# Performance work log

Hardware: AMD Instinct MI355X
Metric: run time of the kernel (lower is better)

## Reference

```python
import jax, jax.numpy as jnp
import numpy as np

TEMPERATURE = 0.1
EPS = 1e-12  # matches F.normalize eps clamp


def setup_inputs() -> dict:
    key = jax.random.key(0)
    k1, k2 = jax.random.split(key)
    B, D = 4096, 1024
    z1 = jax.random.normal(k1, (B, D), dtype=jnp.float32)
    z2 = jax.random.normal(k2, (B, D), dtype=jnp.float32)
    return {"z1": z1, "z2": z2}


def reference(z1, z2):
    B = z1.shape[0]
    # L2-normalize rows (F.normalize dim=1, eps clamp)
    n1 = z1 / jnp.maximum(jnp.linalg.norm(z1, axis=1, keepdims=True), EPS)
    n2 = z2 / jnp.maximum(jnp.linalg.norm(z2, axis=1, keepdims=True), EPS)
    reps = jnp.concatenate([n1, n2], axis=0)  # [2B, D]
    # Rows are unit-norm, so cosine similarity == dot product -> one GEMM
    sim = (reps @ reps.T) / TEMPERATURE  # [2B, 2B]
    # positives: diag offsets +B and -B
    pos = jnp.concatenate([jnp.diagonal(sim, B), jnp.diagonal(sim, -B)])  # [2B]
    # logits row i = [pos_i, sim[i, j != i]]. logsumexp over that set =
    # logaddexp(pos_i, logsumexp over the row with the main diagonal removed).
    eye = jnp.eye(2 * B, dtype=bool)
    masked = jnp.where(eye, -jnp.inf, sim)
    lse_neg = jax.scipy.special.logsumexp(masked, axis=1)  # [2B]
    lse = jnp.logaddexp(pos, lse_neg)
    # CrossEntropyLoss with labels==0 -> mean(lse - logit_0) = mean(lse - pos)
    return jnp.mean(lse - pos)
```

## Files before the change

kernel.cpp:

```cpp
#include <hip/hip_runtime.h>

#define D_DIM 1024
#define B_HALF 4096
#define NROWS 8192
#define INV_T8 (10.0f / 256.0f)
#define NKT64 16
#define NBIG 512
#define NBLK 576

typedef float floatx4 __attribute__((ext_vector_type(4)));

#define MFMA8 __builtin_amdgcn_mfma_f32_16x16x32_fp8_fp8
#define AS1 const __attribute__((address_space(1))) unsigned int*
#define AS3 __attribute__((address_space(3))) unsigned int*

__global__ __launch_bounds__(256) void normalize_kernel(
    const float* __restrict__ z1, const float* __restrict__ z2,
    unsigned char* __restrict__ R8, float* __restrict__ S)
{
    const int tid = threadIdx.x;
    const int lane = tid & 63;
    const int row = blockIdx.x * 4 + (tid >> 6);
    const float* src = (row < B_HALF) ? (z1 + (size_t)row * D_DIM)
                                      : (z2 + (size_t)(row - B_HALF) * D_DIM);
    const float4* s4 = (const float4*)src;
    float4 v0 = s4[lane], v1 = s4[64 + lane], v2 = s4[128 + lane], v3 = s4[192 + lane];
    if (lane == 0) S[row] = 0.0f;
    float ss = v0.x*v0.x + v0.y*v0.y + v0.z*v0.z + v0.w*v0.w
             + v1.x*v1.x + v1.y*v1.y + v1.z*v1.z + v1.w*v1.w
             + v2.x*v2.x + v2.y*v2.y + v2.z*v2.z + v2.w*v2.w
             + v3.x*v3.x + v3.y*v3.y + v3.z*v3.z + v3.w*v3.w;
    ss += __shfl_xor(ss, 1);
    ss += __shfl_xor(ss, 2);
    ss += __shfl_xor(ss, 4);
    ss += __shfl_xor(ss, 8);
    ss += __shfl_xor(ss, 16);
    ss += __shfl_xor(ss, 32);
    float scale = 16.0f / fmaxf(sqrtf(ss), 1e-12f);
    int* dst = (int*)(R8 + (size_t)row * D_DIM);
    float4 vv[4] = {v0, v1, v2, v3};
    #pragma unroll
    for (int i = 0; i < 4; ++i) {
        int w = __builtin_amdgcn_cvt_pk_fp8_f32(vv[i].x * scale, vv[i].y * scale, 0, 0);
        w = __builtin_amdgcn_cvt_pk_fp8_f32(vv[i].z * scale, vv[i].w * scale, w, 1);
        dst[i * 64 + lane] = w;
    }
}

__global__ __launch_bounds__(512, 2) void gemm_lse_kernel(
    const unsigned char* __restrict__ R8,
    float* __restrict__ S, float* __restrict__ pos)
{
    __shared__ unsigned char lds8[2][2][256 * 64];

    const int tid = threadIdx.x;
    const int wave = tid >> 6, lane = tid & 63;
    const int lm = lane & 15, lq = lane >> 4;
    const int wm = wave >> 2, wn = wave & 3;
    const int sRow = lane >> 2;
    const int sCol = (lane & 3) ^ ((sRow >> 1) & 3);
    const int gswz = ((lm >> 1) & 3) << 1;
    const int sk0 = (lq ^ gswz) * 8;
    const int sk1 = ((4 + lq) ^ gswz) * 8;

    if (blockIdx.x < NBIG) {
        int t = blockIdx.x;
        #pragma unroll
        for (int i = 0; i < 16; ++i) {
            const int h = 32 * i - (i * (i - 1)) / 2 + 16;
            if (t >= h) ++t;
        }
        int rt = 0;
        while (t >= 32 - rt) { t -= 32 - rt; ++rt; }
        const int ct = rt + t;
        const bool isDiag = (rt == ct);
        const int row0 = rt * 256, col0 = ct * 256;

        const unsigned char* __restrict__ gA = R8 + (size_t)row0 * D_DIM;
        const unsigned char* __restrict__ gB = R8 + (size_t)col0 * D_DIM;

        floatx4 acc[8][4] = {};

#define BSTAGE(d, kk) \
        { _Pragma("unroll") for (int i = 0; i < 2; ++i) { \
            __builtin_amdgcn_global_load_lds( \
              (AS1)(gA + (size_t)(wave * 32 + i * 16 + sRow) * D_DIM + (kk) + sCol * 16), \
              (AS3)(&lds8[d][0][(wave * 32 + i * 16) * 64]), 16, 0, 0); \
            __builtin_amdgcn_global_load_lds( \
              (AS1)(gB + (size_t)(wave * 32 + i * 16 + sRow) * D_DIM + (kk) + sCol * 16), \
              (AS3)(&lds8[d][1][(wave * 32 + i * 16) * 64]), 16, 0, 0); } }

        BSTAGE(0, 0)
        asm volatile("s_waitcnt vmcnt(0)" ::: "memory");
        __builtin_amdgcn_s_barrier();

        for (int kt = 0; kt < NKT64; ++kt) {
            const int buf = kt & 1;
            const unsigned char* As = &lds8[buf][0][0];
            const unsigned char* Bs = &lds8[buf][1][0];
            if (kt + 1 < NKT64) BSTAGE(buf ^ 1, (kt + 1) * 64)

            long af[8][2], bf[4][2];
            #pragma unroll
            for (int mi = 0; mi < 8; ++mi) {
                const int r = (wm * 128 + mi * 16 + lm) * 64;
                af[mi][0] = *(const long*)(As + r + sk0);
                af[mi][1] = *(const long*)(As + r + sk1);
            }
            #pragma unroll
            for (int ni = 0; ni < 4; ++ni) {
                const int r = (wn * 64 + ni * 16 + lm) * 64;
                bf[ni][0] = *(const long*)(Bs + r + sk0);
                bf[ni][1] = *(const long*)(Bs + r + sk1);
            }

            __builtin_amdgcn_s_setprio(1);
            #pragma unroll
            for (int mi = 0; mi < 8; ++mi)
                #pragma unroll
                for (int ni = 0; ni < 4; ++ni) {
                    acc[mi][ni] = MFMA8(af[mi][0], bf[ni][0], acc[mi][ni], 0, 0, 0);
                    acc[mi][ni] = MFMA8(af[mi][1], bf[ni][1], acc[mi][ni], 0, 0, 0);
                }
            __builtin_amdgcn_s_setprio(0);

            asm volatile("s_waitcnt vmcnt(0)" ::: "memory");
            __builtin_amdgcn_s_barrier();
        }

        float* rowsum = (float*)&lds8[0][0][0];
        float* colsum = rowsum + 4 * 256;
        float ecol[4] = {0.0f, 0.0f, 0.0f, 0.0f};
        #pragma unroll
        for (int mi = 0; mi < 8; ++mi) {
            const int rloc = wm * 128 + mi * 16 + lq * 4;
            #pragma unroll
            for (int reg = 0; reg < 4; ++reg) {
                const int gr = row0 + rloc + reg;
                float esum = 0.0f;
                #pragma unroll
                for (int ni = 0; ni < 4; ++ni) {
                    const int gc = col0 + wn * 64 + ni * 16 + lm;
                    float s = acc[mi][ni][reg] * INV_T8;
                    if (gc == gr + B_HALF) { pos[gr] = s; pos[gc] = s; }
                    float e = (gc == gr) ? 0.0f : __expf(s);
                    esum += e;
                    ecol[ni] += e;
                }
                esum += __shfl_xor(esum, 1);
                esum += __shfl_xor(esum, 2);
                esum += __shfl_xor(esum, 4);
                esum += __shfl_xor(esum, 8);
                if (lm == 0) rowsum[wn * 256 + rloc + reg] = esum;
            }
        }
        #pragma unroll
        for (int ni = 0; ni < 4; ++ni) {
            ecol[ni] += __shfl_xor(ecol[ni], 16);
            ecol[ni] += __shfl_xor(ecol[ni], 32);
        }
        if (lq == 0 && !isDiag) {
            #pragma unroll
            for (int ni = 0; ni < 4; ++ni)
                colsum[wm * 256 + wn * 64 + ni * 16 + lm] = ecol[ni];
        }
        __syncthreads();
        if (tid < 256) {
            float rs = rowsum[tid] + rowsum[256 + tid]
                     + rowsum[512 + tid] + rowsum[768 + tid];
            atomicAdd(&S[row0 + tid], rs);
            if (!isDiag) {
                float cs = colsum[tid] + colsum[256 + tid];
                atomicAdd(&S[col0 + tid], cs);
            }
        }
    } else {
        const int s = blockIdx.x - NBIG;
        const int p = s >> 2, qr = (s >> 1) & 1, qc = s & 1;
        const int row0 = (2 * p + qr) * 128;
        const int col0 = (2 * p + 32 + qc) * 128;

        const unsigned char* __restrict__ gA = R8 + (size_t)row0 * D_DIM;
        const unsigned char* __restrict__ gB = R8 + (size_t)col0 * D_DIM;

        floatx4 acc[4][2] = {};

#define SSTAGE(d, kk) \
        { const int m_ = wave >> 2; \
          const unsigned char* g_ = m_ ? gB : gA; \
          const int w_ = wave & 3; \
          _Pragma("unroll") for (int i = 0; i < 2; ++i) { \
            __builtin_amdgcn_global_load_lds( \
              (AS1)(g_ + (size_t)(w_ * 32 + i * 16 + sRow) * D_DIM + (kk) + sCol * 16), \
              (AS3)(&lds8[d][m_][(w_ * 32 + i * 16) * 64]), 16, 0, 0); } }

        SSTAGE(0, 0)
        asm volatile("s_waitcnt vmcnt(0)" ::: "memory");
        __builtin_amdgcn_s_barrier();

        for (int kt = 0; kt < NKT64; ++kt) {
            const int buf = kt & 1;
            const unsigned char* As = &lds8[buf][0][0];
            const unsigned char* Bs = &lds8[buf][1][0];
            if (kt + 1 < NKT64) SSTAGE(buf ^ 1, (kt + 1) * 64)

            long af[4][2], bf[2][2];
            #pragma unroll
            for (int mi = 0; mi < 4; ++mi) {
                const int r = (wm * 64 + mi * 16 + lm) * 64;
                af[mi][0] = *(const long*)(As + r + sk0);
                af[mi][1] = *(const long*)(As + r + sk1);
            }
            #pragma unroll
            for (int ni = 0; ni < 2; ++ni) {
                const int r = (wn * 32 + ni * 16 + lm) * 64;
                bf[ni][0] = *(const long*)(Bs + r + sk0);
                bf[ni][1] = *(const long*)(Bs + r + sk1);
            }

            __builtin_amdgcn_s_setprio(1);
            #pragma unroll
            for (int mi = 0; mi < 4; ++mi)
                #pragma unroll
                for (int ni = 0; ni < 2; ++ni) {
                    acc[mi][ni] = MFMA8(af[mi][0], bf[ni][0], acc[mi][ni], 0, 0, 0);
                    acc[mi][ni] = MFMA8(af[mi][1], bf[ni][1], acc[mi][ni], 0, 0, 0);
                }
            __builtin_amdgcn_s_setprio(0);

            asm volatile("s_waitcnt vmcnt(0)" ::: "memory");
            __builtin_amdgcn_s_barrier();
        }

        float* rowsum = (float*)&lds8[0][0][0];
        float* colsum = rowsum + 4 * 128;
        float ecol[2] = {0.0f, 0.0f};
        #pragma unroll
        for (int mi = 0; mi < 4; ++mi) {
            const int rloc = wm * 64 + mi * 16 + lq * 4;
            #pragma unroll
            for (int reg = 0; reg < 4; ++reg) {
                const int gr = row0 + rloc + reg;
                float esum = 0.0f;
                #pragma unroll
                for (int ni = 0; ni < 2; ++ni) {
                    const int gc = col0 + wn * 32 + ni * 16 + lm;
                    float s = acc[mi][ni][reg] * INV_T8;
                    if (gc == gr + B_HALF) { pos[gr] = s; pos[gc] = s; }
                    float e = __expf(s);
                    esum += e;
                    ecol[ni] += e;
                }
                esum += __shfl_xor(esum, 1);
                esum += __shfl_xor(esum, 2);
                esum += __shfl_xor(esum, 4);
                esum += __shfl_xor(esum, 8);
                if (lm == 0) rowsum[wn * 128 + rloc + reg] = esum;
            }
        }
        #pragma unroll
        for (int ni = 0; ni < 2; ++ni) {
            ecol[ni] += __shfl_xor(ecol[ni], 16);
            ecol[ni] += __shfl_xor(ecol[ni], 32);
        }
        if (lq == 0) {
            #pragma unroll
            for (int ni = 0; ni < 2; ++ni)
                colsum[wm * 128 + wn * 32 + ni * 16 + lm] = ecol[ni];
        }
        __syncthreads();
        if (tid < 128) {
            float rs = rowsum[tid] + rowsum[128 + tid]
                     + rowsum[256 + tid] + rowsum[384 + tid];
            atomicAdd(&S[row0 + tid], rs);
            float cs = colsum[tid] + colsum[128 + tid];
            atomicAdd(&S[col0 + tid], cs);
        }
    }
}

__global__ __launch_bounds__(1024) void finalize_kernel(
    const float* __restrict__ S, const float* __restrict__ pos,
    float* __restrict__ out)
{
    const int tid = threadIdx.x;
    float local = 0.0f;
    #pragma unroll
    for (int i = 0; i < 8; ++i) {
        const int r = i * 1024 + tid;
        local += log1pf(S[r] * __expf(-pos[r]));
    }
    #pragma unroll
    for (int off = 32; off > 0; off >>= 1) local += __shfl_down(local, off);
    __shared__ float ws[16];
    if ((tid & 63) == 0) ws[tid >> 6] = local;
    __syncthreads();
    if (tid == 0) {
        float tot = 0.0f;
        #pragma unroll
        for (int i = 0; i < 16; ++i) tot += ws[i];
        out[0] = tot * (1.0f / 8192.0f);
    }
}

extern "C" void kernel_launch(void* const* d_in, const int* in_sizes, int n_in,
                              void* d_out, int out_size, void* d_ws, size_t ws_size,
                              hipStream_t stream)
{
    const float* z1 = (const float*)d_in[0];
    const float* z2 = (const float*)d_in[1];
    float* out = (float*)d_out;
    char* ws = (char*)d_ws;
    unsigned char* R8 = (unsigned char*)ws;
    float* pos = (float*)(ws + (size_t)8 * 1024 * 1024);
    float* S   = (float*)(ws + (size_t)8 * 1024 * 1024 + 65536);

    normalize_kernel<<<2048, 256, 0, stream>>>(z1, z2, R8, S);
    gemm_lse_kernel<<<NBLK, 512, 0, stream>>>(R8, S, pos);
    finalize_kernel<<<1, 1024, 0, stream>>>(S, pos, out);
}
```

Before: 163.0 us.

## Permute fp8 K layout in normalize so GEMM reads 16-byte LDS fragments

The normalize kernel now writes each row's fp8 bytes in a permuted K order, so that the two 8-byte MFMA operand halves a lane needs sit next to each other. The GEMM then fetches them with one 16-byte LDS read per fragment instead of two 8-byte reads. The swizzle is simplified to match. This halves the LDS read instruction count in the inner loop. Both operands share the same K permutation, so the dot products are unchanged, but the swizzle must still avoid bank conflicts for the wider reads.

```diff
diff --git a/kernel.cpp b/kernel.cpp
--- a/kernel.cpp
+++ b/kernel.cpp
@@ -9,6 +9,7 @@
 #define NBLK 576
 
 typedef float floatx4 __attribute__((ext_vector_type(4)));
+typedef long longx2 __attribute__((ext_vector_type(2)));
 
 #define MFMA8 __builtin_amdgcn_mfma_f32_16x16x32_fp8_fp8
 #define AS1 const __attribute__((address_space(1))) unsigned int*
@@ -38,12 +39,14 @@
     ss += __shfl_xor(ss, 32);
     float scale = 16.0f / fmaxf(sqrtf(ss), 1e-12f);
     int* dst = (int*)(R8 + (size_t)row * D_DIM);
+    const int dbase = ((lane >> 4) * 16) + (((lane >> 1) & 3) * 4)
+                    + (((lane >> 3) & 1) * 2) + (lane & 1);
     float4 vv[4] = {v0, v1, v2, v3};
     #pragma unroll
     for (int i = 0; i < 4; ++i) {
         int w = __builtin_amdgcn_cvt_pk_fp8_f32(vv[i].x * scale, vv[i].y * scale, 0, 0);
         w = __builtin_amdgcn_cvt_pk_fp8_f32(vv[i].z * scale, vv[i].w * scale, w, 1);
-        dst[i * 64 + lane] = w;
+        dst[i * 64 + dbase] = w;
     }
 }
 
@@ -59,9 +62,7 @@
     const int wm = wave >> 2, wn = wave & 3;
     const int sRow = lane >> 2;
     const int sCol = (lane & 3) ^ ((sRow >> 1) & 3);
-    const int gswz = ((lm >> 1) & 3) << 1;
-    const int sk0 = (lq ^ gswz) * 8;
-    const int sk1 = ((4 + lq) ^ gswz) * 8;
+    const int sk = (lq ^ ((lm >> 1) & 3)) * 16;
 
     if (blockIdx.x < NBIG) {
         int t = blockIdx.x;
@@ -100,19 +101,13 @@
             const unsigned char* Bs = &lds8[buf][1][0];
             if (kt + 1 < NKT64) BSTAGE(buf ^ 1, (kt + 1) * 64)
 
-            long af[8][2], bf[4][2];
-            #pragma unroll
-            for (int mi = 0; mi < 8; ++mi) {
-                const int r = (wm * 128 + mi * 16 + lm) * 64;
-                af[mi][0] = *(const long*)(As + r + sk0);
-                af[mi][1] = *(const long*)(As + r + sk1);
-            }
-            #pragma unroll
-            for (int ni = 0; ni < 4; ++ni) {
-                const int r = (wn * 64 + ni * 16 + lm) * 64;
-                bf[ni][0] = *(const long*)(Bs + r + sk0);
-                bf[ni][1] = *(const long*)(Bs + r + sk1);
-            }
+            longx2 af[8], bf[4];
+            #pragma unroll
+            for (int mi = 0; mi < 8; ++mi)
+                af[mi] = *(const longx2*)(As + (wm * 128 + mi * 16 + lm) * 64 + sk);
+            #pragma unroll
+            for (int ni = 0; ni < 4; ++ni)
+                bf[ni] = *(const longx2*)(Bs + (wn * 64 + ni * 16 + lm) * 64 + sk);
 
             __builtin_amdgcn_s_setprio(1);
             #pragma unroll
@@ -204,19 +199,13 @@
             const unsigned char* Bs = &lds8[buf][1][0];
             if (kt + 1 < NKT64) SSTAGE(buf ^ 1, (kt + 1) * 64)
 
-            long af[4][2], bf[2][2];
-            #pragma unroll
-            for (int mi = 0; mi < 4; ++mi) {
-                const int r = (wm * 64 + mi * 16 + lm) * 64;
-                af[mi][0] = *(const long*)(As + r + sk0);
-                af[mi][1] = *(const long*)(As + r + sk1);
-            }
-            #pragma unroll
-            for (int ni = 0; ni < 2; ++ni) {
-                const int r = (wn * 32 + ni * 16 + lm) * 64;
-                bf[ni][0] = *(const long*)(Bs + r + sk0);
-                bf[ni][1] = *(const long*)(Bs + r + sk1);
-            }
+            longx2 af[4], bf[2];
+            #pragma unroll
+            for (int mi = 0; mi < 4; ++mi)
+                af[mi] = *(const longx2*)(As + (wm * 64 + mi * 16 + lm) * 64 + sk);
+            #pragma unroll
+            for (int ni = 0; ni < 2; ++ni)
+                bf[ni] = *(const longx2*)(Bs + (wn * 32 + ni * 16 + lm) * 64 + sk);
 
             __builtin_amdgcn_s_setprio(1);
             #pragma unroll
```

After: 150.3 us. 7.8% less time.
